# Performance work log

Measured on AMD Instinct MI355X. Metric: run time of the kernel, lower is better.

Reference implementation:

```python
import jax, jax.numpy as jnp
from jax import lax
import numpy as np

LARGE = 1e9  # matches large_number mask sentinel in the torch code
T = 4_194_304


def setup_inputs() -> dict:
    key = jax.random.key(0)
    k1, k2 = jax.random.split(key)
    signal1 = jax.random.normal(k1, (T,), dtype=jnp.float32)
    signal2 = jax.random.normal(k2, (T,), dtype=jnp.float32)
    return {"signal1": signal1, "signal2": signal2, "interval_lo": 0, "interval_hi": 127}


def _until(signal1, signal2, a, b):
    # padding='last': append b+1 copies of the final value
    Tn = signal1.shape[0]
    s1 = jnp.concatenate([signal1, jnp.full((b + 1,), signal1[-1], signal1.dtype)])
    s2 = jnp.concatenate([signal2, jnp.full((b + 1,), signal2[-1], signal2.dtype)])

    def step(carry, delta):
        run_min, run_max = carry
        # running min of s1 over window [j, j+delta]
        run_min = jnp.minimum(run_min, lax.dynamic_slice(s1, (delta,), (Tn,)))
        val = jnp.minimum(run_min, lax.dynamic_slice(s2, (delta,), (Tn,)))
        run_max = jnp.where(delta >= a, jnp.maximum(run_max, val), run_max)
        return (run_min, run_max), None

    init = (jnp.full((Tn,), LARGE, signal1.dtype), jnp.full((Tn,), -LARGE, signal1.dtype))
    (_, out), _ = lax.scan(step, init, jnp.arange(b + 1))
    return out  # out[j] = max_{delta in [a,b]} min(min_{i=j..j+delta} s1[i], s2[j+delta])


def reference(signal1, signal2, interval_lo, interval_hi):
    return _until(signal1, signal2, int(interval_lo), int(interval_hi))
```

## Files before the change

### kernel.cpp

```cpp
#include <hip/hip_runtime.h>

#define LARGEF 1e9f
#define FINF   3.0e38f

constexpr int BLOCK = 256;
constexpr int OPT   = 8;
constexpr int TILE  = BLOCK * OPT;
constexpr int MAXB  = 255;
constexpr int MAXCH = (TILE + MAXB + 31) >> 5;
constexpr int STR   = 36;
constexpr int LDSF  = MAXCH * STR;

__device__ __forceinline__ int pidx(int i) { return (i >> 5) * STR + (i & 31); }

__global__ __launch_bounds__(BLOCK)
void until_kernel(const float* __restrict__ s1, const float* __restrict__ s2,
                  const int* __restrict__ pa, const int* __restrict__ pb,
                  float* __restrict__ out, int T)
{
    const int a = pa[0];
    const int b = pb[0];
    const long base = (long)blockIdx.x * TILE;

    __shared__ float l1[LDSF];
    __shared__ float l2[LDSF];
    __shared__ float cm[LDSF];

    if (b >= 0 && b <= MAXB) {
        const int nch = (TILE + b + 31) >> 5;
        const int Ns  = nch << 5;

        if (base + Ns <= (long)T) {
            for (int i4 = (int)threadIdx.x * 4; i4 < Ns; i4 += BLOCK * 4) {
                float4 u = *(const float4*)(s1 + base + i4);
                float4 v = *(const float4*)(s2 + base + i4);
                *(float4*)&l1[pidx(i4)] = u;
                *(float4*)&l2[pidx(i4)] = v;
            }
        } else {
            for (int i = threadIdx.x; i < Ns; i += BLOCK) {
                long g = base + i; if (g > (long)T - 1) g = (long)T - 1;
                l1[pidx(i)] = s1[g];
                l2[pidx(i)] = s2[g];
            }
        }
        __syncthreads();

        if (a == 0 && b >= 32) {
            if ((int)threadIdx.x < nch) {
                const int cb = (int)threadIdx.x * STR;
                float p = FINF, rm = -FINF;
                #pragma unroll
                for (int q = 0; q < 8; ++q) {
                    float4 u = *(float4*)&l1[cb + q * 4];
                    float4 v = *(float4*)&l2[cb + q * 4];
                    float4 w;
                    p = fminf(p, u.x); rm = fmaxf(rm, fminf(p, v.x)); w.x = rm;
                    p = fminf(p, u.y); rm = fmaxf(rm, fminf(p, v.y)); w.y = rm;
                    p = fminf(p, u.z); rm = fmaxf(rm, fminf(p, v.z)); w.z = rm;
                    p = fminf(p, u.w); rm = fmaxf(rm, fminf(p, v.w)); w.w = rm;
                    *(float4*)&cm[cb + q * 4] = w;
                }
                float smn = FINF, sfn = -FINF;
                #pragma unroll
                for (int q = 7; q >= 0; --q) {
                    float4 u = *(float4*)&l1[cb + q * 4];
                    float4 v = *(float4*)&l2[cb + q * 4];
                    float4 sm4, sf4;
                    sfn = fminf(u.w, fmaxf(v.w, sfn)); sf4.w = sfn;  smn = fminf(u.w, smn); sm4.w = smn;
                    sfn = fminf(u.z, fmaxf(v.z, sfn)); sf4.z = sfn;  smn = fminf(u.z, smn); sm4.z = smn;
                    sfn = fminf(u.y, fmaxf(v.y, sfn)); sf4.y = sfn;  smn = fminf(u.y, smn); sm4.y = smn;
                    sfn = fminf(u.x, fmaxf(v.x, sfn)); sf4.x = sfn;  smn = fminf(u.x, smn); sm4.x = smn;
                    *(float4*)&l1[cb + q * 4] = sm4;
                    *(float4*)&l2[cb + q * 4] = sf4;
                }
            }
            __syncthreads();

            const int jl = (int)threadIdx.x * OPT;
            const int c0 = jl >> 5;
            const int e0 = jl + b;
            const int Gm = e0 >> 5;

            float o[OPT], x[OPT];
            {
                float4 sA = *(float4*)&l2[pidx(jl)];
                float4 sB = *(float4*)&l2[pidx(jl + 4)];
                float4 mA = *(float4*)&l1[pidx(jl)];
                float4 mB = *(float4*)&l1[pidx(jl + 4)];
                o[0]=sA.x; o[1]=sA.y; o[2]=sA.z; o[3]=sA.w;
                o[4]=sB.x; o[5]=sB.y; o[6]=sB.z; o[7]=sB.w;
                x[0]=mA.x; x[1]=mA.y; x[2]=mA.z; x[3]=mA.w;
                x[4]=mB.x; x[5]=mB.y; x[6]=mB.z; x[7]=mB.w;
            }
            for (int g = c0 + 1; g < Gm; ++g) {
                const float GV = cm[g * STR + 31];
                const float WV = l1[g * STR];
                #pragma unroll
                for (int r = 0; r < OPT; ++r) {
                    o[r] = fmaxf(o[r], fminf(x[r], GV));
                    x[r] = fminf(x[r], WV);
                }
            }
            {
                const float GV = cm[Gm * STR + 31];
                const float WV = l1[Gm * STR];
                const int lim = (Gm + 1) << 5;
                #pragma unroll
                for (int r = 0; r < OPT; ++r) {
                    const int e = e0 + r;
                    if (e >= lim) {
                        o[r] = fmaxf(o[r], fminf(x[r], GV));
                        x[r] = fminf(x[r], WV);
                    }
                    o[r] = fmaxf(o[r], fminf(x[r], cm[pidx(e)]));
                }
            }
            const long jg = base + jl;
            if (jg + OPT <= (long)T) {
                *(float4*)(out + jg)     = make_float4(o[0], o[1], o[2], o[3]);
                *(float4*)(out + jg + 4) = make_float4(o[4], o[5], o[6], o[7]);
            } else {
                for (int r = 0; r < OPT; ++r)
                    if (jg + r < (long)T) out[jg + r] = o[r];
            }
        } else {
            const int j0 = (int)threadIdx.x * OPT;
            float m[OPT], o[OPT];
            #pragma unroll
            for (int r = 0; r < OPT; ++r) { m[r] = LARGEF; o[r] = -LARGEF; }
            for (int k = 0; k <= b + OPT - 1; ++k) {
                const float v1 = l1[pidx(j0 + k)];
                const float v2 = l2[pidx(j0 + k)];
                #pragma unroll
                for (int r = 0; r < OPT; ++r) {
                    const int d = k - r;
                    if (d >= 0 && d <= b) {
                        m[r] = fminf(m[r], v1);
                        if (d >= a) o[r] = fmaxf(o[r], fminf(m[r], v2));
                    }
                }
            }
            const long jg = base + j0;
            if (jg + OPT <= (long)T) {
                *(float4*)(out + jg)     = make_float4(o[0], o[1], o[2], o[3]);
                *(float4*)(out + jg + 4) = make_float4(o[4], o[5], o[6], o[7]);
            } else {
                for (int r = 0; r < OPT; ++r)
                    if (jg + r < (long)T) out[jg + r] = o[r];
            }
        }
    } else {
        const long j0 = base + (long)threadIdx.x * OPT;
        float m[OPT], o[OPT];
        #pragma unroll
        for (int r = 0; r < OPT; ++r) { m[r] = LARGEF; o[r] = -LARGEF; }
        const long kend = (long)b + OPT - 1;
        for (long k = 0; k <= kend; ++k) {
            long g = j0 + k;
            if (g > (long)T - 1) g = (long)T - 1;
            if (g < 0) g = 0;
            const float v1 = s1[g];
            const float v2 = s2[g];
            #pragma unroll
            for (int r = 0; r < OPT; ++r) {
                const long d = k - r;
                if (d >= 0 && d <= (long)b) {
                    m[r] = fminf(m[r], v1);
                    if (d >= (long)a) o[r] = fmaxf(o[r], fminf(m[r], v2));
                }
            }
        }
        for (int r = 0; r < OPT; ++r)
            if (j0 + r < (long)T) out[j0 + r] = o[r];
    }
}

extern "C" void kernel_launch(void* const* d_in, const int* in_sizes, int n_in,
                              void* d_out, int out_size, void* d_ws, size_t ws_size,
                              hipStream_t stream) {
    const float* s1 = (const float*)d_in[0];
    const float* s2 = (const float*)d_in[1];
    const int*   pa = (const int*)d_in[2];
    const int*   pb = (const int*)d_in[3];
    float* out = (float*)d_out;
    const int T = in_sizes[0];

    const int nblk = (T + TILE - 1) / TILE;
    until_kernel<<<nblk, BLOCK, 0, stream>>>(s1, s2, pa, pb, out, T);
}
```

Before: 89.86 us.

## Use van Herk-style block prefix/suffix combine for aligned window sizes

```diff
diff --git a/kernel.cpp b/kernel.cpp
--- a/kernel.cpp
+++ b/kernel.cpp
@@ -10,6 +10,7 @@
 constexpr int MAXCH = (TILE + MAXB + 31) >> 5;
 constexpr int STR   = 36;
 constexpr int LDSF  = MAXCH * STR;
+constexpr int SUMN  = 68;
 
 __device__ __forceinline__ int pidx(int i) { return (i >> 5) * STR + (i & 31); }
 
@@ -21,24 +22,28 @@
     const int a = pa[0];
     const int b = pb[0];
     const long base = (long)blockIdx.x * TILE;
+    const int tid = (int)threadIdx.x;
 
     __shared__ float l1[LDSF];
     __shared__ float l2[LDSF];
     __shared__ float cm[LDSF];
+    __shared__ float Psum[SUMN], Rsum[SUMN];
+    __shared__ float PpA[SUMN], RpA[SUMN];
+    __shared__ float MsA[SUMN], RsA[SUMN];
 
     if (b >= 0 && b <= MAXB) {
         const int nch = (TILE + b + 31) >> 5;
         const int Ns  = nch << 5;
 
         if (base + Ns <= (long)T) {
-            for (int i4 = (int)threadIdx.x * 4; i4 < Ns; i4 += BLOCK * 4) {
+            for (int i4 = tid * 4; i4 < Ns; i4 += BLOCK * 4) {
                 float4 u = *(const float4*)(s1 + base + i4);
                 float4 v = *(const float4*)(s2 + base + i4);
                 *(float4*)&l1[pidx(i4)] = u;
                 *(float4*)&l2[pidx(i4)] = v;
             }
         } else {
-            for (int i = threadIdx.x; i < Ns; i += BLOCK) {
+            for (int i = tid; i < Ns; i += BLOCK) {
                 long g = base + i; if (g > (long)T - 1) g = (long)T - 1;
                 l1[pidx(i)] = s1[g];
                 l2[pidx(i)] = s2[g];
@@ -46,9 +51,12 @@
         }
         __syncthreads();
 
-        if (a == 0 && b >= 32) {
-            if ((int)threadIdx.x < nch) {
-                const int cb = (int)threadIdx.x * STR;
+        const bool vh = (a == 0) && (b == 31 || b == 63 || b == 127);
+
+        if (vh) {
+
+            if (tid < nch) {
+                const int cb = tid * STR;
                 float p = FINF, rm = -FINF;
                 #pragma unroll
                 for (int q = 0; q < 8; ++q) {
@@ -74,10 +82,109 @@
                     *(float4*)&l1[cb + q * 4] = sm4;
                     *(float4*)&l2[cb + q * 4] = sf4;
                 }
+                Psum[tid] = smn;
+                Rsum[tid] = rm;
             }
             __syncthreads();
 
-            const int jl = (int)threadIdx.x * OPT;
+            const int cpl = (b + 1) >> 5;
+            const int nLb = (64 / cpl) + 1;
+            if (tid < nLb) {
+                const int cb = tid * cpl;
+                float Pp = FINF, Rp = -FINF;
+                for (int i = 0; i < cpl; ++i) {
+                    const int c = cb + i;
+                    PpA[c] = Pp; RpA[c] = Rp;
+                    const float P = Psum[c], R = Rsum[c];
+                    Rp = fmaxf(Rp, fminf(Pp, R));
+                    Pp = fminf(Pp, P);
+                }
+                float Ms = FINF, Rs = -FINF;
+                for (int i = cpl - 1; i >= 0; --i) {
+                    const int c = cb + i;
+                    MsA[c] = Ms; RsA[c] = Rs;
+                    const float P = Psum[c], R = Rsum[c];
+                    Rs = fmaxf(R, fminf(P, Rs));
+                    Ms = fminf(P, Ms);
+                }
+            }
+            __syncthreads();
+
+            const int jl = tid * OPT;
+            const int c0 = jl >> 5;
+            const float Ms = MsA[c0], Rs = RsA[c0];
+
+            float sf[OPT], sm[OPT];
+            {
+                float4 fA = *(float4*)&l2[pidx(jl)];
+                float4 fB = *(float4*)&l2[pidx(jl + 4)];
+                float4 mA = *(float4*)&l1[pidx(jl)];
+                float4 mB = *(float4*)&l1[pidx(jl + 4)];
+                sf[0]=fA.x; sf[1]=fA.y; sf[2]=fA.z; sf[3]=fA.w;
+                sf[4]=fB.x; sf[5]=fB.y; sf[6]=fB.z; sf[7]=fB.w;
+                sm[0]=mA.x; sm[1]=mA.y; sm[2]=mA.z; sm[3]=mA.w;
+                sm[4]=mB.x; sm[5]=mB.y; sm[6]=mB.z; sm[7]=mB.w;
+            }
+
+            const int e0 = jl + b;
+            const int celo = e0 >> 5;
+            const int cehi = (e0 + OPT - 1) >> 5;
+            const float Pl = PpA[celo], Rl = RpA[celo];
+            const float Ph = PpA[cehi], Rh = RpA[cehi];
+
+            float o[OPT];
+            #pragma unroll
+            for (int r = 0; r < OPT; ++r) {
+                const int e = e0 + r;
+                const bool hi = (e >> 5) != celo;
+                const float Pp = hi ? Ph : Pl;
+                const float Rp = hi ? Rh : Rl;
+                const float cme = fmaxf(Rp, fminf(Pp, cm[pidx(e)]));
+                const float SUF = fmaxf(sf[r], fminf(sm[r], Rs));
+                const float SM  = fminf(sm[r], Ms);
+                o[r] = fmaxf(SUF, fminf(SM, cme));
+            }
+
+            const long jg = base + jl;
+            if (jg + OPT <= (long)T) {
+                *(float4*)(out + jg)     = make_float4(o[0], o[1], o[2], o[3]);
+                *(float4*)(out + jg + 4) = make_float4(o[4], o[5], o[6], o[7]);
+            } else {
+                for (int r = 0; r < OPT; ++r)
+                    if (jg + r < (long)T) out[jg + r] = o[r];
+            }
+        } else if (a == 0 && b >= 32) {
+            if (tid < nch) {
+                const int cb = tid * STR;
+                float p = FINF, rm = -FINF;
+                #pragma unroll
+                for (int q = 0; q < 8; ++q) {
+                    float4 u = *(float4*)&l1[cb + q * 4];
+                    float4 v = *(float4*)&l2[cb + q * 4];
+                    float4 w;
+                    p = fminf(p, u.x); rm = fmaxf(rm, fminf(p, v.x)); w.x = rm;
+                    p = fminf(p, u.y); rm = fmaxf(rm, fminf(p, v.y)); w.y = rm;
+                    p = fminf(p, u.z); rm = fmaxf(rm, fminf(p, v.z)); w.z = rm;
+                    p = fminf(p, u.w); rm = fmaxf(rm, fminf(p, v.w)); w.w = rm;
+                    *(float4*)&cm[cb + q * 4] = w;
+                }
+                float smn = FINF, sfn = -FINF;
+                #pragma unroll
+                for (int q = 7; q >= 0; --q) {
+                    float4 u = *(float4*)&l1[cb + q * 4];
+                    float4 v = *(float4*)&l2[cb + q * 4];
+                    float4 sm4, sf4;
+                    sfn = fminf(u.w, fmaxf(v.w, sfn)); sf4.w = sfn;  smn = fminf(u.w, smn); sm4.w = smn;
+                    sfn = fminf(u.z, fmaxf(v.z, sfn)); sf4.z = sfn;  smn = fminf(u.z, smn); sm4.z = smn;
+                    sfn = fminf(u.y, fmaxf(v.y, sfn)); sf4.y = sfn;  smn = fminf(u.y, smn); sm4.y = smn;
+                    sfn = fminf(u.x, fmaxf(v.x, sfn)); sf4.x = sfn;  smn = fminf(u.x, smn); sm4.x = smn;
+                    *(float4*)&l1[cb + q * 4] = sm4;
+                    *(float4*)&l2[cb + q * 4] = sf4;
+                }
+            }
+            __syncthreads();
+
+            const int jl = tid * OPT;
             const int c0 = jl >> 5;
             const int e0 = jl + b;
             const int Gm = e0 >> 5;
@@ -125,7 +232,7 @@
                     if (jg + r < (long)T) out[jg + r] = o[r];
             }
         } else {
-            const int j0 = (int)threadIdx.x * OPT;
+            const int j0 = tid * OPT;
             float m[OPT], o[OPT];
             #pragma unroll
             for (int r = 0; r < OPT; ++r) { m[r] = LARGEF; o[r] = -LARGEF; }
@@ -151,7 +258,7 @@
             }
         }
     } else {
-        const long j0 = base + (long)threadIdx.x * OPT;
+        const long j0 = base + (long)tid * OPT;
         float m[OPT], o[OPT];
         #pragma unroll
         for (int r = 0; r < OPT; ++r) { m[r] = LARGEF; o[r] = -LARGEF; }
```

Measured after the change: 91.77 us. 1.02x slower.

## Add aligned-window fast path using wavefront shuffle scans for power-of-two windows

Applied to the files above, without the earlier changes.

```diff
diff --git a/kernel.cpp b/kernel.cpp
--- a/kernel.cpp
+++ b/kernel.cpp
@@ -21,24 +21,149 @@
     const int a = pa[0];
     const int b = pb[0];
     const long base = (long)blockIdx.x * TILE;
+    const int tid = (int)threadIdx.x;
 
     __shared__ float l1[LDSF];
     __shared__ float l2[LDSF];
     __shared__ float cm[LDSF];
 
+    const bool vh = (a == 0) && (b == 31 || b == 63 || b == 127);
+
+    if (vh) {
+        float* cmArr = l1;
+        const int G   = (b + 1) >> 3;
+        const int gm  = G - 1;
+        const int lane = tid & 63;
+        const int lig  = lane & gm;
+
+        float u[OPT], v[OPT];
+        const long jg = base + (long)tid * OPT;
+        if (base + TILE <= (long)T) {
+            float4 uA = *(const float4*)(s1 + jg);
+            float4 uB = *(const float4*)(s1 + jg + 4);
+            float4 vA = *(const float4*)(s2 + jg);
+            float4 vB = *(const float4*)(s2 + jg + 4);
+            u[0]=uA.x;u[1]=uA.y;u[2]=uA.z;u[3]=uA.w;u[4]=uB.x;u[5]=uB.y;u[6]=uB.z;u[7]=uB.w;
+            v[0]=vA.x;v[1]=vA.y;v[2]=vA.z;v[3]=vA.w;v[4]=vB.x;v[5]=vB.y;v[6]=vB.z;v[7]=vB.w;
+        } else {
+            #pragma unroll
+            for (int k = 0; k < OPT; ++k) {
+                long g = jg + k; if (g > (long)T - 1) g = (long)T - 1;
+                u[k] = s1[g]; v[k] = s2[g];
+            }
+        }
+
+        float cmR[OPT], smL[OPT], sfL[OPT];
+        float p = FINF, r0 = -FINF;
+        #pragma unroll
+        for (int k = 0; k < OPT; ++k) {
+            p  = fminf(p, u[k]);
+            r0 = fmaxf(r0, fminf(p, v[k]));
+            cmR[k] = r0;
+        }
+        float smv = FINF, sfv = -FINF;
+        #pragma unroll
+        for (int k = OPT - 1; k >= 0; --k) {
+            sfv = fminf(u[k], fmaxf(v[k], sfv));
+            smv = fminf(u[k], smv);
+            smL[k] = smv; sfL[k] = sfv;
+        }
+
+        float Pi = p, Ri = r0;
+        for (int d = 1; d < G; d <<= 1) {
+            float Pu = __shfl_up(Pi, d);
+            float Ru = __shfl_up(Ri, d);
+            if (lig >= d) { Ri = fmaxf(Ru, fminf(Pu, Ri)); Pi = fminf(Pu, Pi); }
+        }
+        float Pp = __shfl_up(Pi, 1), Rp = __shfl_up(Ri, 1);
+        if (lig == 0) { Pp = FINF; Rp = -FINF; }
+
+        float Ps = p, Rs = r0;
+        for (int d = 1; d < G; d <<= 1) {
+            float Pd = __shfl_down(Ps, d);
+            float Rd = __shfl_down(Rs, d);
+            if (lig + d < G) { Rs = fmaxf(Rs, fminf(Ps, Rd)); Ps = fminf(Ps, Pd); }
+        }
+        float Ms = __shfl_down(Ps, 1), Re = __shfl_down(Rs, 1);
+        if (lig == gm) { Ms = FINF; Re = -FINF; }
+
+        const int jl = tid * OPT;
+        {
+            float4 cA, cB;
+            cA.x = fmaxf(Rp, fminf(Pp, cmR[0]));
+            cA.y = fmaxf(Rp, fminf(Pp, cmR[1]));
+            cA.z = fmaxf(Rp, fminf(Pp, cmR[2]));
+            cA.w = fmaxf(Rp, fminf(Pp, cmR[3]));
+            cB.x = fmaxf(Rp, fminf(Pp, cmR[4]));
+            cB.y = fmaxf(Rp, fminf(Pp, cmR[5]));
+            cB.z = fmaxf(Rp, fminf(Pp, cmR[6]));
+            cB.w = fmaxf(Rp, fminf(Pp, cmR[7]));
+            *(float4*)&cmArr[jl]     = cA;
+            *(float4*)&cmArr[jl + 4] = cB;
+        }
+
+        if (tid < 64) {
+            float hu[OPT], hv[OPT], hcm[OPT];
+            const long hb = base + TILE + (long)lig * OPT;
+            #pragma unroll
+            for (int k = 0; k < OPT; ++k) {
+                long g = hb + k; if (g > (long)T - 1) g = (long)T - 1;
+                hu[k] = s1[g]; hv[k] = s2[g];
+            }
+            float hp = FINF, hr = -FINF;
+            #pragma unroll
+            for (int k = 0; k < OPT; ++k) {
+                hp = fminf(hp, hu[k]);
+                hr = fmaxf(hr, fminf(hp, hv[k]));
+                hcm[k] = hr;
+            }
+            float hPi = hp, hRi = hr;
+            for (int d = 1; d < G; d <<= 1) {
+                float Pu = __shfl_up(hPi, d);
+                float Ru = __shfl_up(hRi, d);
+                if (lig >= d) { hRi = fmaxf(Ru, fminf(Pu, hRi)); hPi = fminf(Pu, hPi); }
+            }
+            float hPp = __shfl_up(hPi, 1), hRp = __shfl_up(hRi, 1);
+            if (lig == 0) { hPp = FINF; hRp = -FINF; }
+            if (lane < G) {
+                #pragma unroll
+                for (int k = 0; k < OPT; ++k)
+                    cmArr[TILE + lane * OPT + k] = fmaxf(hRp, fminf(hPp, hcm[k]));
+            }
+        }
+        __syncthreads();
+
+        float o[OPT];
+        #pragma unroll
+        for (int k = 0; k < OPT; ++k) {
+            const float E   = cmArr[jl + k + b];
+            const float SUF = fmaxf(sfL[k], fminf(smL[k], Re));
+            const float SMv = fminf(smL[k], Ms);
+            o[k] = fmaxf(SUF, fminf(SMv, E));
+        }
+        if (jg + OPT <= (long)T) {
+            *(float4*)(out + jg)     = make_float4(o[0], o[1], o[2], o[3]);
+            *(float4*)(out + jg + 4) = make_float4(o[4], o[5], o[6], o[7]);
+        } else {
+            for (int k = 0; k < OPT; ++k)
+                if (jg + k < (long)T) out[jg + k] = o[k];
+        }
+        return;
+    }
+
     if (b >= 0 && b <= MAXB) {
         const int nch = (TILE + b + 31) >> 5;
         const int Ns  = nch << 5;
 
         if (base + Ns <= (long)T) {
-            for (int i4 = (int)threadIdx.x * 4; i4 < Ns; i4 += BLOCK * 4) {
-                float4 u = *(const float4*)(s1 + base + i4);
-                float4 v = *(const float4*)(s2 + base + i4);
-                *(float4*)&l1[pidx(i4)] = u;
-                *(float4*)&l2[pidx(i4)] = v;
+            for (int i4 = tid * 4; i4 < Ns; i4 += BLOCK * 4) {
+                float4 uu = *(const float4*)(s1 + base + i4);
+                float4 vv = *(const float4*)(s2 + base + i4);
+                *(float4*)&l1[pidx(i4)] = uu;
+                *(float4*)&l2[pidx(i4)] = vv;
             }
         } else {
-            for (int i = threadIdx.x; i < Ns; i += BLOCK) {
+            for (int i = tid; i < Ns; i += BLOCK) {
                 long g = base + i; if (g > (long)T - 1) g = (long)T - 1;
                 l1[pidx(i)] = s1[g];
                 l2[pidx(i)] = s2[g];
@@ -47,37 +172,37 @@
         __syncthreads();
 
         if (a == 0 && b >= 32) {
-            if ((int)threadIdx.x < nch) {
-                const int cb = (int)threadIdx.x * STR;
+            if (tid < nch) {
+                const int cb = tid * STR;
                 float p = FINF, rm = -FINF;
                 #pragma unroll
                 for (int q = 0; q < 8; ++q) {
-                    float4 u = *(float4*)&l1[cb + q * 4];
-                    float4 v = *(float4*)&l2[cb + q * 4];
+                    float4 uu = *(float4*)&l1[cb + q * 4];
+                    float4 vv = *(float4*)&l2[cb + q * 4];
                     float4 w;
-                    p = fminf(p, u.x); rm = fmaxf(rm, fminf(p, v.x)); w.x = rm;
-                    p = fminf(p, u.y); rm = fmaxf(rm, fminf(p, v.y)); w.y = rm;
-                    p = fminf(p, u.z); rm = fmaxf(rm, fminf(p, v.z)); w.z = rm;
-                    p = fminf(p, u.w); rm = fmaxf(rm, fminf(p, v.w)); w.w = rm;
+                    p = fminf(p, uu.x); rm = fmaxf(rm, fminf(p, vv.x)); w.x = rm;
+                    p = fminf(p, uu.y); rm = fmaxf(rm, fminf(p, vv.y)); w.y = rm;
+                    p = fminf(p, uu.z); rm = fmaxf(rm, fminf(p, vv.z)); w.z = rm;
+                    p = fminf(p, uu.w); rm = fmaxf(rm, fminf(p, vv.w)); w.w = rm;
                     *(float4*)&cm[cb + q * 4] = w;
                 }
                 float smn = FINF, sfn = -FINF;
                 #pragma unroll
                 for (int q = 7; q >= 0; --q) {
-                    float4 u = *(float4*)&l1[cb + q * 4];
-                    float4 v = *(float4*)&l2[cb + q * 4];
+                    float4 uu = *(float4*)&l1[cb + q * 4];
+                    float4 vv = *(float4*)&l2[cb + q * 4];
                     float4 sm4, sf4;
-                    sfn = fminf(u.w, fmaxf(v.w, sfn)); sf4.w = sfn;  smn = fminf(u.w, smn); sm4.w = smn;
-                    sfn = fminf(u.z, fmaxf(v.z, sfn)); sf4.z = sfn;  smn = fminf(u.z, smn); sm4.z = smn;
-                    sfn = fminf(u.y, fmaxf(v.y, sfn)); sf4.y = sfn;  smn = fminf(u.y, smn); sm4.y = smn;
-                    sfn = fminf(u.x, fmaxf(v.x, sfn)); sf4.x = sfn;  smn = fminf(u.x, smn); sm4.x = smn;
+                    sfn = fminf(uu.w, fmaxf(vv.w, sfn)); sf4.w = sfn;  smn = fminf(uu.w, smn); sm4.w = smn;
+                    sfn = fminf(uu.z, fmaxf(vv.z, sfn)); sf4.z = sfn;  smn = fminf(uu.z, smn); sm4.z = smn;
+                    sfn = fminf(uu.y, fmaxf(vv.y, sfn)); sf4.y = sfn;  smn = fminf(uu.y, smn); sm4.y = smn;
+                    sfn = fminf(uu.x, fmaxf(vv.x, sfn)); sf4.x = sfn;  smn = fminf(uu.x, smn); sm4.x = smn;
                     *(float4*)&l1[cb + q * 4] = sm4;
                     *(float4*)&l2[cb + q * 4] = sf4;
                 }
             }
             __syncthreads();
 
-            const int jl = (int)threadIdx.x * OPT;
+            const int jl = tid * OPT;
             const int c0 = jl >> 5;
             const int e0 = jl + b;
             const int Gm = e0 >> 5;
@@ -116,16 +241,16 @@
                     o[r] = fmaxf(o[r], fminf(x[r], cm[pidx(e)]));
                 }
             }
-            const long jg = base + jl;
-            if (jg + OPT <= (long)T) {
-                *(float4*)(out + jg)     = make_float4(o[0], o[1], o[2], o[3]);
-                *(float4*)(out + jg + 4) = make_float4(o[4], o[5], o[6], o[7]);
+            const long jgo = base + jl;
+            if (jgo + OPT <= (long)T) {
+                *(float4*)(out + jgo)     = make_float4(o[0], o[1], o[2], o[3]);
+                *(float4*)(out + jgo + 4) = make_float4(o[4], o[5], o[6], o[7]);
             } else {
                 for (int r = 0; r < OPT; ++r)
-                    if (jg + r < (long)T) out[jg + r] = o[r];
+                    if (jgo + r < (long)T) out[jgo + r] = o[r];
             }
         } else {
-            const int j0 = (int)threadIdx.x * OPT;
+            const int j0 = tid * OPT;
             float m[OPT], o[OPT];
             #pragma unroll
             for (int r = 0; r < OPT; ++r) { m[r] = LARGEF; o[r] = -LARGEF; }
@@ -141,17 +266,17 @@
                     }
                 }
             }
-            const long jg = base + j0;
-            if (jg + OPT <= (long)T) {
-                *(float4*)(out + jg)     = make_float4(o[0], o[1], o[2], o[3]);
-                *(float4*)(out + jg + 4) = make_float4(o[4], o[5], o[6], o[7]);
+            const long jgo = base + j0;
+            if (jgo + OPT <= (long)T) {
+                *(float4*)(out + jgo)     = make_float4(o[0], o[1], o[2], o[3]);
+                *(float4*)(out + jgo + 4) = make_float4(o[4], o[5], o[6], o[7]);
             } else {
                 for (int r = 0; r < OPT; ++r)
-                    if (jg + r < (long)T) out[jg + r] = o[r];
+                    if (jgo + r < (long)T) out[jgo + r] = o[r];
             }
         }
     } else {
-        const long j0 = base + (long)threadIdx.x * OPT;
+        const long j0 = base + (long)tid * OPT;
         float m[OPT], o[OPT];
         #pragma unroll
         for (int r = 0; r < OPT; ++r) { m[r] = LARGEF; o[r] = -LARGEF; }
```

Measured after the change: 86.56 us. 1.04x faster.
